# Performance work log

Measured on AMD Instinct MI355X. Metric: run time of the kernel, lower is better.

The kernel has to match this reference:

```python
import jax, jax.numpy as jnp
import numpy as np

B, T, C, H = 4, 4096, 1024, 128

def setup_inputs() -> dict:
    key = jax.random.key(0)
    k1, k2, k3, k4 = jax.random.split(key, 4)
    x = jax.random.normal(k1, (B, T, C), dtype=jnp.float32)
    # nn.Linear(embed, head, bias=False): y = x @ W, store W as [C, H]
    s = 1.0 / np.sqrt(C)
    Wk = jax.random.normal(k2, (C, H), dtype=jnp.float32) * s
    Wq = jax.random.normal(k3, (C, H), dtype=jnp.float32) * s
    Wv = jax.random.normal(k4, (C, H), dtype=jnp.float32) * s
    return {"x": x, "Wk": Wk, "Wq": Wq, "Wv": Wv}

def reference(x, Wk, Wq, Wv):
    Bx, Tx, Cx = x.shape
    scale = Wk.shape[1] ** -0.5
    k = x @ Wk  # [B,T,H]
    q = x @ Wq
    v = x @ Wv
    att = jnp.einsum('bth,bsh->bts', q, k) * scale  # [B,T,T]
    causal = jnp.triu(jnp.ones((Tx, Tx), dtype=bool), k=1)
    att = jnp.where(causal, -jnp.inf, att)
    att = jax.nn.softmax(att, axis=-1)
    # dropout is identity in eval mode
    out = jnp.einsum('bts,bsh->bth', att, v)  # [B,T,H]
    return out
```

## Files before the change

kernel.cpp:

```cpp
#include <hip/hip_runtime.h>
#include <stdint.h>
#include <math.h>

#define B_ 4
#define T_ 4096
#define C_ 1024
#define H_ 128

typedef __attribute__((ext_vector_type(8))) short s16x8;
typedef __attribute__((ext_vector_type(4))) float f32x4;

__device__ __forceinline__ unsigned short f2bf(float f) {
    union { float f; unsigned u; } v; v.f = f;
    unsigned r = v.u + 0x7fffu + ((v.u >> 16) & 1u);
    return (unsigned short)(r >> 16);
}

__device__ __forceinline__ s16x8 as_frag(uint4 u) {
    union { uint4 u; s16x8 s; } v; v.u = u; return v.s;
}

__host__ __device__ constexpr int chunks128(int CH) {
    int H2 = CH / 2;
    int k = 32 / H2, r = 32 % H2;
    return H2 * k * (k + 1) / 2 + r * (k + 1);
}

#define QSC (0.0883883476f * 1.4426950408f)

__global__ __launch_bounds__(256) void k_wt(const float* __restrict__ Wk,
                                            const float* __restrict__ Wq,
                                            const float* __restrict__ Wv,
                                            unsigned short* __restrict__ Wt) {
    __shared__ float tile[64][65];
    int w = blockIdx.z;
    const float* W = (w == 0) ? Wk : (w == 1) ? Wq : Wv;
    int c0 = blockIdx.x * 64, h0 = blockIdx.y * 64;
    int tid = threadIdx.x;
#pragma unroll
    for (int k = 0; k < 16; k++) {
        int idx = tid + k * 256;
        int r = idx >> 6, c = idx & 63;
        tile[r][c] = W[(size_t)(c0 + r) * H_ + h0 + c];
    }
    __syncthreads();
#pragma unroll
    for (int k = 0; k < 16; k++) {
        int idx = tid + k * 256;
        int hh = idx >> 6, cc = idx & 63;
        Wt[(size_t)(w * H_ + h0 + hh) * C_ + c0 + cc] = f2bf(tile[cc][hh]);
    }
}

__global__ __launch_bounds__(256, 3) void k_qkv(const float* __restrict__ x,
                                                const unsigned short* __restrict__ Wt,
                                                unsigned short* __restrict__ Qb,
                                                unsigned short* __restrict__ Kb,
                                                unsigned short* __restrict__ Vt) {
    __shared__ unsigned short a_lds[2][64 * 72];
    int tid = threadIdx.x;
    int wv = tid >> 6, lane = tid & 63, quad = lane >> 4, lo = lane & 15;
    int r0 = blockIdx.x * 64;
    int cb = blockIdx.y;
    int nt0 = wv * 3;

    f32x4 acc[3][4];
#pragma unroll
    for (int i = 0; i < 3; i++)
#pragma unroll
        for (int j = 0; j < 4; j++) acc[i][j] = (f32x4){0.f, 0.f, 0.f, 0.f};

    const int row_s = tid >> 2;
    const int seg_s = (tid & 3) * 16;
    size_t xbase = (size_t)(r0 + row_s) * C_ + seg_s;

    const unsigned short* wp[3];
#pragma unroll
    for (int nt = 0; nt < 3; nt++)
        wp[nt] = Wt + (size_t)(cb * 192 + (nt0 + nt) * 16 + lo) * C_ + quad * 8;

    auto pack_store = [&](unsigned short* buf, const float4 (&f)[4]) {
        uint4 u0, u1;
        u0.x = (unsigned)f2bf(f[0].x) | ((unsigned)f2bf(f[0].y) << 16);
        u0.y = (unsigned)f2bf(f[0].z) | ((unsigned)f2bf(f[0].w) << 16);
        u0.z = (unsigned)f2bf(f[1].x) | ((unsigned)f2bf(f[1].y) << 16);
        u0.w = (unsigned)f2bf(f[1].z) | ((unsigned)f2bf(f[1].w) << 16);
        u1.x = (unsigned)f2bf(f[2].x) | ((unsigned)f2bf(f[2].y) << 16);
        u1.y = (unsigned)f2bf(f[2].z) | ((unsigned)f2bf(f[2].w) << 16);
        u1.z = (unsigned)f2bf(f[3].x) | ((unsigned)f2bf(f[3].y) << 16);
        u1.w = (unsigned)f2bf(f[3].z) | ((unsigned)f2bf(f[3].w) << 16);
        *(uint4*)&buf[row_s * 72 + seg_s] = u0;
        *(uint4*)&buf[row_s * 72 + seg_s + 8] = u1;
    };
    auto load_x = [&](float4 (&f)[4], int kc) {
        const float* xp = x + xbase + kc * 64;
#pragma unroll
        for (int j = 0; j < 4; j++) f[j] = *(const float4*)(xp + j * 4);
    };

    float4 xr[4];
    load_x(xr, 0);
    pack_store(a_lds[0], xr);
    __syncthreads();

    for (int kc = 0; kc < 16; kc++) {
        const unsigned short* buf = a_lds[kc & 1];
        float4 xn[4];
        if (kc < 15) load_x(xn, kc + 1);
        s16x8 b[3][2];
#pragma unroll
        for (int nt = 0; nt < 3; nt++)
#pragma unroll
            for (int kh = 0; kh < 2; kh++)
                b[nt][kh] = *(const s16x8*)(wp[nt] + kc * 64 + kh * 32);
        s16x8 af[4][2];
#pragma unroll
        for (int mt = 0; mt < 4; mt++)
#pragma unroll
            for (int kh = 0; kh < 2; kh++)
                af[mt][kh] = *(const s16x8*)&buf[(mt * 16 + lo) * 72 + kh * 32 + quad * 8];
#pragma unroll
        for (int nt = 0; nt < 3; nt++)
#pragma unroll
            for (int kh = 0; kh < 2; kh++)
#pragma unroll
                for (int mt = 0; mt < 4; mt++)
                    acc[nt][mt] = __builtin_amdgcn_mfma_f32_16x16x32_bf16(
                        af[mt][kh], b[nt][kh], acc[nt][mt], 0, 0, 0);
        if (kc < 15) pack_store((unsigned short*)a_lds[(kc & 1) ^ 1], xn);
        __syncthreads();
    }

#pragma unroll
    for (int nt = 0; nt < 3; nt++) {
        int col = cb * 192 + (nt0 + nt) * 16 + lo;
        int w = col >> 7, h = col & 127;
#pragma unroll
        for (int mt = 0; mt < 4; mt++) {
            int mrow = r0 + mt * 16 + quad * 4;
            if (w == 2) {
                int b = mrow >> 12, t0 = mrow & 4095;
                int tp = (t0 & ~31) + (((t0 & 15) >> 2) << 3) + (((t0 >> 4) & 1) << 2);
                uint2 pk;
                pk.x = (unsigned)f2bf(acc[nt][mt][0]) | ((unsigned)f2bf(acc[nt][mt][1]) << 16);
                pk.y = (unsigned)f2bf(acc[nt][mt][2]) | ((unsigned)f2bf(acc[nt][mt][3]) << 16);
                *(uint2*)(Vt + (size_t)(b * H_ + h) * T_ + tp) = pk;
            } else if (w == 1) {
                unsigned short* dst = Qb + (size_t)mrow * H_ + h;
#pragma unroll
                for (int r = 0; r < 4; r++)
                    dst[(size_t)r * H_] = f2bf(acc[nt][mt][r] * QSC);
            } else {
                unsigned short* dst = Kb + (size_t)mrow * H_ + h;
#pragma unroll
                for (int r = 0; r < 4; r++)
                    dst[(size_t)r * H_] = f2bf(acc[nt][mt][r]);
            }
        }
    }
}

#define LOAD_KV(kv0)                                                            \
    do {                                                                        \
        const uint4* kg = (const uint4*)(Kb + (size_t)(batch * T_ + (kv0) + srow_k) * H_); \
        pk0 = kg[sseg_k + 0]; pk1 = kg[sseg_k + 1];                             \
        const uint4* vg = (const uint4*)(Vt + (size_t)(batch * H_ + srow_v) * T_ + (kv0)); \
        pv0 = vg[sseg_v + 0]; pv1 = vg[sseg_v + 1];                             \
    } while (0)

template <int CH>
__global__ __launch_bounds__(512, 4) void k_attn(const unsigned short* __restrict__ Qb,
                                                 const unsigned short* __restrict__ Kb,
                                                 const unsigned short* __restrict__ Vt,
                                                 float* __restrict__ Opart,
                                                 float* __restrict__ Mpart,
                                                 float* __restrict__ Lpart) {
    __shared__ uint4 kbuf[64 * 16];
    __shared__ uint4 vbuf[128 * 8];

    int tid = threadIdx.x;
    int wv = tid >> 6, lane = tid & 63, quad = lane >> 4, lo = lane & 15;

    int id = blockIdx.x;
    int batch = id & 3;
    int slot = id >> 2;
    int s = slot, q = 31;
    for (;;) { int nc = (2 * q + 1 + CH) / CH; if (s < nc) break; s -= nc; --q; }
    int qb = q;
    int tbeg = s * CH;
    int tend = min(tbeg + CH, 2 * qb + 2);
    int m0 = qb * 128 + wv * 16;
    int query = m0 + lo;

    s16x8 qf[4];
    size_t qrow = (size_t)(batch * T_ + m0 + lo) * H_;
#pragma unroll
    for (int ks = 0; ks < 4; ks++)
        qf[ks] = *(const s16x8*)(Qb + qrow + ks * 32 + quad * 8);

    f32x4 acc_o[8];
#pragma unroll
    for (int o = 0; o < 8; o++) acc_o[o] = (f32x4){0.f, 0.f, 0.f, 0.f};
    float m_i = -INFINITY, l_i = 0.f;

    const int srow_k = tid >> 3, sseg_k = (tid & 7) * 2;
    const int srow_v = tid >> 2, sseg_v = (tid & 3) * 2;

    uint4 pk0, pk1, pv0, pv1;
    LOAD_KV(tbeg * 64);

    for (int t = tbeg; t < tend; ++t) {
        int kv0 = t * 64;
        kbuf[srow_k * 16 + ((sseg_k + 0) ^ (srow_k & 15))] = pk0;
        kbuf[srow_k * 16 + ((sseg_k + 1) ^ (srow_k & 15))] = pk1;
        vbuf[srow_v * 8 + ((sseg_v + 0) ^ (srow_v & 7))] = pv0;
        vbuf[srow_v * 8 + ((sseg_v + 1) ^ (srow_v & 7))] = pv1;
        __syncthreads();
        if (t + 1 < tend) LOAD_KV((t + 1) * 64);

        f32x4 s_acc[4];
#pragma unroll
        for (int nt = 0; nt < 4; nt++) s_acc[nt] = (f32x4){0.f, 0.f, 0.f, 0.f};
        __builtin_amdgcn_s_setprio(1);
#pragma unroll
        for (int ks = 0; ks < 4; ks++) {
#pragma unroll
            for (int nt = 0; nt < 4; nt++) {
                s16x8 kf = as_frag(kbuf[(nt * 16 + lo) * 16 + ((ks * 4 + quad) ^ lo)]);
                s_acc[nt] = __builtin_amdgcn_mfma_f32_16x16x32_bf16(kf, qf[ks], s_acc[nt], 0, 0, 0);
            }
        }
        __builtin_amdgcn_s_setprio(0);

        float p[4][4];
#pragma unroll
        for (int nt = 0; nt < 4; nt++)
#pragma unroll
            for (int r = 0; r < 4; r++) p[nt][r] = s_acc[nt][r];
        if (kv0 + 63 > m0) {
#pragma unroll
            for (int nt = 0; nt < 4; nt++)
#pragma unroll
                for (int r = 0; r < 4; r++)
                    if (kv0 + nt * 16 + quad * 4 + r > query) p[nt][r] = -INFINITY;
        }

        float mx = p[0][0];
#pragma unroll
        for (int nt = 0; nt < 4; nt++)
#pragma unroll
            for (int r = 0; r < 4; r++) mx = fmaxf(mx, p[nt][r]);
        if (__any(mx > m_i + 8.0f)) {
            float rm = fmaxf(mx, __shfl_xor(mx, 16));
            rm = fmaxf(rm, __shfl_xor(rm, 32));
            float mnew = fmaxf(m_i, rm);
            float alpha = exp2f(m_i - mnew);
            l_i *= alpha;
            m_i = mnew;
#pragma unroll
            for (int o = 0; o < 8; o++)
#pragma unroll
                for (int r = 0; r < 4; r++) acc_o[o][r] *= alpha;
        }
        float rs = 0.f;
#pragma unroll
        for (int nt = 0; nt < 4; nt++)
#pragma unroll
            for (int r = 0; r < 4; r++) {
                float pv = exp2f(p[nt][r] - m_i);
                p[nt][r] = pv;
                rs += pv;
            }
        l_i += rs;

        s16x8 pf[2];
#pragma unroll
        for (int kt = 0; kt < 2; kt++) {
            uint4 u;
            u.x = (__float_as_uint(p[2 * kt][0]) >> 16) | ((__float_as_uint(p[2 * kt][1]) >> 16) << 16);
            u.y = (__float_as_uint(p[2 * kt][2]) >> 16) | ((__float_as_uint(p[2 * kt][3]) >> 16) << 16);
            u.z = (__float_as_uint(p[2 * kt + 1][0]) >> 16) | ((__float_as_uint(p[2 * kt + 1][1]) >> 16) << 16);
            u.w = (__float_as_uint(p[2 * kt + 1][2]) >> 16) | ((__float_as_uint(p[2 * kt + 1][3]) >> 16) << 16);
            pf[kt] = as_frag(u);
        }

        __builtin_amdgcn_s_setprio(1);
#pragma unroll
        for (int kt = 0; kt < 2; kt++)
#pragma unroll
            for (int o = 0; o < 8; o++) {
                int vrow = o * 16 + lo;
                s16x8 vf = as_frag(vbuf[vrow * 8 + ((kt * 4 + quad) ^ (vrow & 7))]);
                acc_o[o] = __builtin_amdgcn_mfma_f32_16x16x32_bf16(vf, pf[kt], acc_o[o], 0, 0, 0);
            }
        __builtin_amdgcn_s_setprio(0);
        __syncthreads();
    }

    l_i += __shfl_xor(l_i, 16);
    l_i += __shfl_xor(l_i, 32);

    constexpr int NCH = chunks128(CH);
    size_t pr = (size_t)(batch * NCH + slot) * 128 + wv * 16 + lo;
    float* Op = Opart + pr * 128;
#pragma unroll
    for (int o = 0; o < 8; o++) {
        float4 v = {acc_o[o][0], acc_o[o][1], acc_o[o][2], acc_o[o][3]};
        *(float4*)(Op + o * 16 + quad * 4) = v;
    }
    if (quad == 0) { Mpart[pr] = m_i; Lpart[pr] = l_i; }
}

template <int CH>
__global__ __launch_bounds__(256) void k_comb(const float* __restrict__ Opart,
                                              const float* __restrict__ Mpart,
                                              const float* __restrict__ Lpart,
                                              float* __restrict__ out) {
    constexpr int NCH = chunks128(CH);
    constexpr int H2 = CH / 2;
    int tid = threadIdx.x;
    int row = blockIdx.x * 8 + (tid >> 5);
    int h4 = (tid & 31) * 4;
    int batch = row >> 12, t = row & 4095, qb = t >> 7, rr = t & 127;
    int nc = (2 * qb + 1 + CH) / CH;
    int n = qb + 1, k = n / H2, r = n % H2;
    int F = H2 * k * (k + 1) / 2 + r * (k + 1);
    int base = NCH - F;
    float M = -INFINITY, den = 0.f;
    float4 o = {0.f, 0.f, 0.f, 0.f};
    for (int s = 0; s < nc; ++s) {
        size_t pr = (size_t)(batch * NCH + base + s) * 128 + rr;
        float ms = Mpart[pr], ls = Lpart[pr];
        float4 v = *(const float4*)(Opart + pr * 128 + h4);
        float Mn = fmaxf(M, ms);
        float wa = exp2f(M - Mn), wb = exp2f(ms - Mn);
        den = den * wa + ls * wb;
        o.x = o.x * wa + v.x * wb;
        o.y = o.y * wa + v.y * wb;
        o.z = o.z * wa + v.z * wb;
        o.w = o.w * wa + v.w * wb;
        M = Mn;
    }
    float inv = 1.0f / den;
    float4 rz = {o.x * inv, o.y * inv, o.z * inv, o.w * inv};
    *(float4*)(out + (size_t)row * H_ + h4) = rz;
}

extern "C" void kernel_launch(void* const* d_in, const int* in_sizes, int n_in,
                              void* d_out, int out_size, void* d_ws, size_t ws_size,
                              hipStream_t stream) {
    const float* x  = (const float*)d_in[0];
    const float* Wk = (const float*)d_in[1];
    const float* Wq = (const float*)d_in[2];
    const float* Wv = (const float*)d_in[3];
    char* ws = (char*)d_ws;
    unsigned short* Wt = (unsigned short*)ws;
    unsigned short* Qb = (unsigned short*)(ws + (1u << 20));
    unsigned short* Kb = (unsigned short*)(ws + (5u << 20));
    unsigned short* Vt = (unsigned short*)(ws + (9u << 20));
    float* out = (float*)d_out;

    const size_t base = (size_t)13 << 20;
    constexpr int N10 = chunks128(10);
    constexpr int N20 = chunks128(20);
    auto need_for = [&](int nch) {
        return base + (size_t)4 * nch * 128 * (128 * 4) + 2 * (size_t)4 * nch * 128 * 4;
    };

    k_wt  <<<dim3(16, 2, 3), 256, 0, stream>>>(Wk, Wq, Wv, Wt);
    k_qkv <<<dim3(256, 2), 256, 0, stream>>>(x, Wt, Qb, Kb, Vt);

    if (ws_size >= need_for(N10)) {
        float* Op = (float*)(ws + base);
        float* Mp = Op + (size_t)4 * N10 * 128 * 128;
        float* Lp = Mp + (size_t)4 * N10 * 128;
        k_attn<10><<<4 * N10, 512, 0, stream>>>(Qb, Kb, Vt, Op, Mp, Lp);
        k_comb<10><<<2048, 256, 0, stream>>>(Op, Mp, Lp, out);
    } else {
        float* Op = (float*)(ws + base);
        float* Mp = Op + (size_t)4 * N20 * 128 * 128;
        float* Lp = Mp + (size_t)4 * N20 * 128;
        k_attn<20><<<4 * N20, 512, 0, stream>>>(Qb, Kb, Vt, Op, Mp, Lp);
        k_comb<20><<<2048, 256, 0, stream>>>(Op, Mp, Lp, out);
    }
}
```

Before: 162.0 us.

## Write unsplit attention rows directly, store partials in bf16, shrink chunk size

When a query block's KV range fits in one chunk, the attention kernel now normalizes and writes the final output directly, and the combine kernel skips those rows. Partial outputs for split rows are stored as bf16 instead of fp32, halving partial-buffer traffic, and the split-KV chunk size drops from 10 to 8 (20 to 16 in the fallback). Together these aim to cut workspace write/read bandwidth and combine work. The trade-off is extra rounding error in the partial accumulators and more blocks from the smaller chunk size.

```diff
diff --git a/kernel.cpp b/kernel.cpp
--- a/kernel.cpp
+++ b/kernel.cpp
@@ -14,6 +14,10 @@
     union { float f; unsigned u; } v; v.f = f;
     unsigned r = v.u + 0x7fffu + ((v.u >> 16) & 1u);
     return (unsigned short)(r >> 16);
+}
+
+__device__ __forceinline__ float bf2f(unsigned short s) {
+    union { unsigned u; float f; } v; v.u = (unsigned)s << 16; return v.f;
 }
 
 __device__ __forceinline__ s16x8 as_frag(uint4 u) {
@@ -172,9 +176,10 @@
 __global__ __launch_bounds__(512, 4) void k_attn(const unsigned short* __restrict__ Qb,
                                                  const unsigned short* __restrict__ Kb,
                                                  const unsigned short* __restrict__ Vt,
-                                                 float* __restrict__ Opart,
+                                                 unsigned short* __restrict__ Opart,
                                                  float* __restrict__ Mpart,
-                                                 float* __restrict__ Lpart) {
+                                                 float* __restrict__ Lpart,
+                                                 float* __restrict__ out) {
     __shared__ uint4 kbuf[64 * 16];
     __shared__ uint4 vbuf[128 * 8];
 
@@ -300,19 +305,33 @@
     l_i += __shfl_xor(l_i, 16);
     l_i += __shfl_xor(l_i, 32);
 
-    constexpr int NCH = chunks128(CH);
-    size_t pr = (size_t)(batch * NCH + slot) * 128 + wv * 16 + lo;
-    float* Op = Opart + pr * 128;
-#pragma unroll
-    for (int o = 0; o < 8; o++) {
-        float4 v = {acc_o[o][0], acc_o[o][1], acc_o[o][2], acc_o[o][3]};
-        *(float4*)(Op + o * 16 + quad * 4) = v;
-    }
-    if (quad == 0) { Mpart[pr] = m_i; Lpart[pr] = l_i; }
+    bool direct = (tbeg == 0) && (tend == 2 * qb + 2);
+    if (direct) {
+        float inv = 1.0f / l_i;
+        int rowg = batch * T_ + m0 + lo;
+#pragma unroll
+        for (int o = 0; o < 8; o++) {
+            float4 v = {acc_o[o][0] * inv, acc_o[o][1] * inv,
+                        acc_o[o][2] * inv, acc_o[o][3] * inv};
+            *(float4*)(out + (size_t)rowg * H_ + o * 16 + quad * 4) = v;
+        }
+    } else {
+        constexpr int NCH = chunks128(CH);
+        size_t pr = (size_t)(batch * NCH + slot) * 128 + wv * 16 + lo;
+        unsigned short* Op = Opart + pr * 128;
+#pragma unroll
+        for (int o = 0; o < 8; o++) {
+            uint2 pk;
+            pk.x = (unsigned)f2bf(acc_o[o][0]) | ((unsigned)f2bf(acc_o[o][1]) << 16);
+            pk.y = (unsigned)f2bf(acc_o[o][2]) | ((unsigned)f2bf(acc_o[o][3]) << 16);
+            *(uint2*)(Op + o * 16 + quad * 4) = pk;
+        }
+        if (quad == 0) { Mpart[pr] = m_i; Lpart[pr] = l_i; }
+    }
 }
 
 template <int CH>
-__global__ __launch_bounds__(256) void k_comb(const float* __restrict__ Opart,
+__global__ __launch_bounds__(256) void k_comb(const unsigned short* __restrict__ Opart,
                                               const float* __restrict__ Mpart,
                                               const float* __restrict__ Lpart,
                                               float* __restrict__ out) {
@@ -323,6 +342,7 @@
     int h4 = (tid & 31) * 4;
     int batch = row >> 12, t = row & 4095, qb = t >> 7, rr = t & 127;
     int nc = (2 * qb + 1 + CH) / CH;
+    if (nc == 1) return;
     int n = qb + 1, k = n / H2, r = n % H2;
     int F = H2 * k * (k + 1) / 2 + r * (k + 1);
     int base = NCH - F;
@@ -331,7 +351,11 @@
     for (int s = 0; s < nc; ++s) {
         size_t pr = (size_t)(batch * NCH + base + s) * 128 + rr;
         float ms = Mpart[pr], ls = Lpart[pr];
-        float4 v = *(const float4*)(Opart + pr * 128 + h4);
+        uint2 u = *(const uint2*)(Opart + pr * 128 + h4);
+        float4 v = {bf2f((unsigned short)(u.x & 0xffff)),
+                    bf2f((unsigned short)(u.x >> 16)),
+                    bf2f((unsigned short)(u.y & 0xffff)),
+                    bf2f((unsigned short)(u.y >> 16))};
         float Mn = fmaxf(M, ms);
         float wa = exp2f(M - Mn), wb = exp2f(ms - Mn);
         den = den * wa + ls * wb;
@@ -361,26 +385,26 @@
     float* out = (float*)d_out;
 
     const size_t base = (size_t)13 << 20;
-    constexpr int N10 = chunks128(10);
-    constexpr int N20 = chunks128(20);
+    constexpr int N8  = chunks128(8);
+    constexpr int N16 = chunks128(16);
     auto need_for = [&](int nch) {
-        return base + (size_t)4 * nch * 128 * (128 * 4) + 2 * (size_t)4 * nch * 128 * 4;
+        return base + (size_t)4 * nch * 128 * (128 * 2) + 2 * (size_t)4 * nch * 128 * 4;
     };
 
     k_wt  <<<dim3(16, 2, 3), 256, 0, stream>>>(Wk, Wq, Wv, Wt);
     k_qkv <<<dim3(256, 2), 256, 0, stream>>>(x, Wt, Qb, Kb, Vt);
 
-    if (ws_size >= need_for(N10)) {
-        float* Op = (float*)(ws + base);
-        float* Mp = Op + (size_t)4 * N10 * 128 * 128;
-        float* Lp = Mp + (size_t)4 * N10 * 128;
-        k_attn<10><<<4 * N10, 512, 0, stream>>>(Qb, Kb, Vt, Op, Mp, Lp);
-        k_comb<10><<<2048, 256, 0, stream>>>(Op, Mp, Lp, out);
+    if (ws_size >= need_for(N8)) {
+        unsigned short* Op = (unsigned short*)(ws + base);
+        float* Mp = (float*)(ws + base + (size_t)4 * N8 * 128 * 256);
+        float* Lp = Mp + (size_t)4 * N8 * 128;
+        k_attn<8><<<4 * N8, 512, 0, stream>>>(Qb, Kb, Vt, Op, Mp, Lp, out);
+        k_comb<8><<<2048, 256, 0, stream>>>(Op, Mp, Lp, out);
     } else {
-        float* Op = (float*)(ws + base);
-        float* Mp = Op + (size_t)4 * N20 * 128 * 128;
-        float* Lp = Mp + (size_t)4 * N20 * 128;
-        k_attn<20><<<4 * N20, 512, 0, stream>>>(Qb, Kb, Vt, Op, Mp, Lp);
-        k_comb<20><<<2048, 256, 0, stream>>>(Op, Mp, Lp, out);
-    }
-}
+        unsigned short* Op = (unsigned short*)(ws + base);
+        float* Mp = (float*)(ws + base + (size_t)4 * N16 * 128 * 256);
+        float* Lp = Mp + (size_t)4 * N16 * 128;
+        k_attn<16><<<4 * N16, 512, 0, stream>>>(Qb, Kb, Vt, Op, Mp, Lp, out);
+        k_comb<16><<<2048, 256, 0, stream>>>(Op, Mp, Lp, out);
+    }
+}
```

Result: slower. 166.7 us (+2.9%).
